# Optimization experiments

Measured on AMD Instinct MI355X. Metric: run time of the kernel, lower is better.

## Reference

```python
import jax, jax.numpy as jnp
import numpy as np

B, T, E = 4, 2048, 768
HN, HS = 12, 64          # head_num, head_size = E // HN
L = 6                    # n_layer
FF = 4 * E
O = 1                    # output_dim
EPS = 1e-5


def setup_inputs() -> dict:
    key = jax.random.key(0)
    ks = iter(jax.random.split(key, 40))
    r = lambda shape, s=0.02: jax.random.normal(next(ks), shape, jnp.float32) * s
    inp = {
        'idx': jax.random.normal(next(ks), (B, T, E), jnp.float32),
        'hidden': jnp.zeros((1, B, E), jnp.float32),
        # per-layer, per-head q/k/v linears
        'wq': r((L, HN, E, HS)), 'bq': jnp.zeros((L, HN, HS), jnp.float32),
        'wk': r((L, HN, E, HS)), 'bk': jnp.zeros((L, HN, HS), jnp.float32),
        'wv': r((L, HN, E, HS)), 'bv': jnp.zeros((L, HN, HS), jnp.float32),
        'wproj': r((L, E, E)), 'bproj': jnp.zeros((L, E), jnp.float32),
        'ln1_g': jnp.ones((L, E), jnp.float32), 'ln1_b': jnp.zeros((L, E), jnp.float32),
        'ln2_g': jnp.ones((L, E), jnp.float32), 'ln2_b': jnp.zeros((L, E), jnp.float32),
        'w1': r((L, E, FF)), 'b1': jnp.zeros((L, FF), jnp.float32),
        'w2': r((L, FF, E)), 'b2': jnp.zeros((L, E), jnp.float32),
        'lnf_g': jnp.ones((E,), jnp.float32), 'lnf_b': jnp.zeros((E,), jnp.float32),
        'fw1': r((E, FF)), 'fb1': jnp.zeros((FF,), jnp.float32),
        'fw2': r((FF, E)), 'fb2': jnp.zeros((E,), jnp.float32),
        'hw': r((E, O)), 'hb': jnp.zeros((O,), jnp.float32),
    }
    return inp


def _layernorm(x, g, b):
    m = jnp.mean(x, axis=-1, keepdims=True)
    v = jnp.var(x, axis=-1, keepdims=True)
    return (x - m) * jax.lax.rsqrt(v + EPS) * g + b


def _forward(idx, wq, bq, wk, bk, wv, bv, wproj, bproj,
             ln1_g, ln1_b, ln2_g, ln2_b, w1, b1, w2, b2,
             lnf_g, lnf_b, fw1, fb1, fw2, fb2, hw, hb):
    x = idx
    Bn, Tn, En = x.shape
    causal = jnp.tril(jnp.ones((Tn, Tn), bool))  # [T,T]
    scale = 1.0 / jnp.sqrt(jnp.asarray(En, x.dtype))  # NOTE: divides by sqrt(n_embed), as in source
    for l in range(wq.shape[0]):
        h = _layernorm(x, ln1_g[l], ln1_b[l])
        q = jnp.einsum('bte,hes->bhts', h, wq[l]) + bq[l][None, :, None, :]
        k = jnp.einsum('bte,hes->bhts', h, wk[l]) + bk[l][None, :, None, :]
        v = jnp.einsum('bte,hes->bhts', h, wv[l]) + bv[l][None, :, None, :]
        scores = jnp.einsum('bhts,bhus->bhtu', q, k) * scale
        scores = jnp.where(causal, scores, -jnp.inf)
        att = jax.nn.softmax(scores, axis=-1)
        o = jnp.einsum('bhtu,bhus->bhts', att, v)          # [B,HN,T,HS]
        o = o.transpose(0, 2, 1, 3).reshape(Bn, Tn, En)     # concat heads
        x = x + o @ wproj[l] + bproj[l]
        h = _layernorm(x, ln2_g[l], ln2_b[l])
        ff = jax.nn.gelu(h @ w1[l] + b1[l], approximate=False) @ w2[l] + b2[l]
        x = x + ff
    x = _layernorm(x, lnf_g, lnf_b)
    x = jax.nn.gelu(x @ fw1 + fb1, approximate=False) @ fw2 + fb2
    logits = x @ hw + hb            # [B,T,O]
    logits = logits[-1]             # [T,O]  (source: logits[-1,:,:])
    return jnp.squeeze(logits, axis=-1)  # [T]


def reference(idx, hidden, wq, bq, wk, bk, wv, bv, wproj, bproj,
              ln1_g, ln1_b, ln2_g, ln2_b, w1, b1, w2, b2,
              lnf_g, lnf_b, fw1, fb1, fw2, fb2, hw, hb):
    # hidden is accepted but unused by the original module.
    del hidden
    return _forward(idx, wq, bq, wk, bk, wv, bv, wproj, bproj,
                    ln1_g, ln1_b, ln2_g, ln2_b, w1, b1, w2, b2,
                    lnf_g, lnf_b, fw1, fb1, fw2, fb2, hw, hb)
```

## Files before the change

kernel.cpp:

```cpp
#include <hip/hip_runtime.h>
#include <math.h>

#define TT 2048
#define EE 768
#define HNN 12
#define HSS 64
#define NLAYER 6
#define FFD 3072
#define QKVN 2304

constexpr float LN_EPS = 1e-5f;
constexpr float ATT_SCALE = 0.03608439182435161f;

typedef __attribute__((ext_vector_type(8))) short bf16x8;
typedef __attribute__((ext_vector_type(4))) float f32x4;

__device__ __forceinline__ ushort f2bf(float f) {
    union { float f; uint u; } c; c.f = f;
    const uint u = c.u;
    return (ushort)((u + 0x7fffu + ((u >> 16) & 1u)) >> 16);
}

__device__ __forceinline__ void gload16(const void* g, void* l) {
    __builtin_amdgcn_global_load_lds((const __attribute__((address_space(1))) void*)g,
                                     (__attribute__((address_space(3))) void*)l, 16, 0, 0);
}

__global__ __launch_bounds__(256) void copy4_kernel(float4* __restrict__ dst,
                                                    const float4* __restrict__ src, int n4) {
    int i = blockIdx.x * 256 + threadIdx.x;
    if (i < n4) dst[i] = src[i];
}

__global__ __launch_bounds__(256) void ln_kernel(const float* __restrict__ in,
                                                 const float* __restrict__ g,
                                                 const float* __restrict__ b,
                                                 ushort* __restrict__ out) {
    __shared__ float red[8];
    const int t = blockIdx.x;
    const int tid = threadIdx.x;
    const float* row = in + (size_t)t * EE;
    float v0 = row[tid], v1 = row[tid + 256], v2 = row[tid + 512];
    float s = v0 + v1 + v2;
#pragma unroll
    for (int m = 1; m < 64; m <<= 1) s += __shfl_xor(s, m, 64);
    if ((tid & 63) == 0) red[tid >> 6] = s;
    __syncthreads();
    const float mean = (red[0] + red[1] + red[2] + red[3]) * (1.0f / EE);
    const float d0 = v0 - mean, d1 = v1 - mean, d2 = v2 - mean;
    float qq = d0 * d0 + d1 * d1 + d2 * d2;
#pragma unroll
    for (int m = 1; m < 64; m <<= 1) qq += __shfl_xor(qq, m, 64);
    __syncthreads();
    if ((tid & 63) == 0) red[tid >> 6] = qq;
    __syncthreads();
    const float var = (red[0] + red[1] + red[2] + red[3]) * (1.0f / EE);
    const float rstd = rsqrtf(var + LN_EPS);
    ushort* orow = out + (size_t)t * EE;
    orow[tid]       = f2bf(d0 * rstd * g[tid]       + b[tid]);
    orow[tid + 256] = f2bf(d1 * rstd * g[tid + 256] + b[tid + 256]);
    orow[tid + 512] = f2bf(d2 * rstd * g[tid + 512] + b[tid + 512]);
}

__device__ __forceinline__ void transpose64(const float* __restrict__ src, int sld,
                                            ushort* __restrict__ dst, int dld,
                                            int k0, int n0, int tid) {
    __shared__ float t[64][68];
#pragma unroll
    for (int p = 0; p < 4; p++) {
        const int kr = p * 16 + (tid >> 4);
        *(float4*)&t[kr][(tid & 15) * 4] =
            *(const float4*)&src[(size_t)(k0 + kr) * sld + n0 + (tid & 15) * 4];
    }
    __syncthreads();
#pragma unroll
    for (int q = 0; q < 2; q++) {
        const int nl = q * 32 + (tid >> 3);
        const int kc = (tid & 7) * 8;
        ushort v[8];
#pragma unroll
        for (int j = 0; j < 8; j++) v[j] = f2bf(t[kc + j][nl]);
        uint4 o;
        o.x = (uint)v[0] | ((uint)v[1] << 16);
        o.y = (uint)v[2] | ((uint)v[3] << 16);
        o.z = (uint)v[4] | ((uint)v[5] << 16);
        o.w = (uint)v[6] | ((uint)v[7] << 16);
        *(uint4*)&dst[(size_t)(n0 + nl) * dld + k0 + kc] = o;
    }
}

__global__ __launch_bounds__(256) void pack_t_kernel(const float* __restrict__ src, int sld,
                                                     ushort* __restrict__ dst, int dld) {
    transpose64(src, sld, dst, dld, blockIdx.x * 64, blockIdx.y * 64, threadIdx.x);
}

__global__ __launch_bounds__(256) void pack_qkv_kernel(const float* __restrict__ wq,
                                                       const float* __restrict__ wk,
                                                       const float* __restrict__ wv,
                                                       ushort* __restrict__ dst) {
    const int z = blockIdx.z;
    const int which = z / HNN, hd = z % HNN;
    const float* src = (which == 0 ? wq : which == 1 ? wk : wv) + (size_t)hd * EE * HSS;
    ushort* d = dst + (size_t)(which * EE + hd * HSS) * EE;
    transpose64(src, HSS, d, EE, blockIdx.x * 64, 0, threadIdx.x);
}

template <int EPI>
__global__ __launch_bounds__(256) void gemm_bf16(const ushort* __restrict__ A,
                                                 const ushort* __restrict__ Bt,
                                                 const float* __restrict__ b0,
                                                 const float* __restrict__ b1,
                                                 const float* __restrict__ b2,
                                                 float* __restrict__ outF,
                                                 ushort* __restrict__ outB,
                                                 int N, int K,
                                                 int nby, int KS, int Kslice) {
    __shared__ ushort Al[2][128 * 32];
    __shared__ ushort Bl[2][128 * 32];
    const int tid = threadIdx.x;
    const int wave = tid >> 6, lane = tid & 63;
    const int wm = wave >> 1, wn = wave & 1;
    const int l15 = lane & 15, q4 = lane >> 4;

    const int nwg = gridDim.x;
    const int wgid = ((int)blockIdx.x & 7) * (nwg >> 3) + ((int)blockIdx.x >> 3);
    const int mb = wgid % nby;
    const int t2 = wgid / nby;
    const int ks = t2 % KS;
    const int nb = t2 / KS;
    const int m0 = mb * 128, n0 = nb * 128;
    const int kbase = ks * Kslice;

    const int srow = lane >> 2;
    const int scb = (lane & 3) ^ ((lane >> 3) & 3);
    const ushort* Ag0 = A + (size_t)(m0 + wave * 16 + srow) * K + kbase + scb * 8;
    const ushort* Ag1 = Ag0 + (size_t)64 * K;
    const ushort* Bg0 = Bt + (size_t)(n0 + wave * 16 + srow) * K + kbase + scb * 8;
    const ushort* Bg1 = Bg0 + (size_t)64 * K;

    auto stage = [&](int buf, int kk) {
        const int off = kk * 32;
        gload16(Ag0 + off, &Al[buf][(wave * 16) * 32]);
        gload16(Ag1 + off, &Al[buf][(64 + wave * 16) * 32]);
        gload16(Bg0 + off, &Bl[buf][(wave * 16) * 32]);
        gload16(Bg1 + off, &Bl[buf][(64 + wave * 16) * 32]);
    };

    f32x4 acc[4][4];
#pragma unroll
    for (int i = 0; i < 4; i++)
#pragma unroll
        for (int j = 0; j < 4; j++) acc[i][j] = (f32x4){0.f, 0.f, 0.f, 0.f};

    stage(0, 0);
    __syncthreads();

    const int niter = Kslice >> 5;
    const int cq = (q4 ^ ((l15 >> 1) & 3)) * 8;

    for (int i = 0; i < niter; i++) {
        const int buf = i & 1;
        if (i + 1 < niter) stage(buf ^ 1, i + 1);
        bf16x8 af[4], bfr[4];
#pragma unroll
        for (int ii = 0; ii < 4; ii++)
            af[ii] = *(const bf16x8*)&Al[buf][(wm * 64 + ii * 16 + l15) * 32 + cq];
#pragma unroll
        for (int j = 0; j < 4; j++)
            bfr[j] = *(const bf16x8*)&Bl[buf][(wn * 64 + j * 16 + l15) * 32 + cq];
#pragma unroll
        for (int ii = 0; ii < 4; ii++)
#pragma unroll
            for (int j = 0; j < 4; j++)
                acc[ii][j] = __builtin_amdgcn_mfma_f32_16x16x32_bf16(af[ii], bfr[j], acc[ii][j], 0, 0, 0);
        __syncthreads();
    }

#pragma unroll
    for (int i = 0; i < 4; i++) {
        const int row = m0 + wm * 64 + i * 16 + q4 * 4;
#pragma unroll
        for (int j = 0; j < 4; j++) {
            const int col = n0 + wn * 64 + j * 16 + l15;
            float bias;
            if constexpr (EPI == 0)
                bias = (col < 768) ? b0[col] : (col < 1536 ? b1[col - 768] : b2[col - 1536]);
            else
                bias = (EPI == 1 && ks != 0) ? 0.f : b0[col];
#pragma unroll
            for (int r = 0; r < 4; r++) {
                const float v = acc[i][j][r] + bias;
                const size_t idx = (size_t)(row + r) * N + col;
                if constexpr (EPI == 0) {
                    outB[idx] = f2bf(v);
                } else if constexpr (EPI == 1) {
                    atomicAdd(&outF[idx], v);
                } else if constexpr (EPI == 2) {
                    outB[idx] = f2bf(0.5f * v * (1.0f + erff(v * 0.70710678118654752f)));
                } else {
                    outF[idx] = v;
                }
            }
        }
    }
}

__global__ __launch_bounds__(256) void attn_mfma(const ushort* __restrict__ qkv,
                                                 ushort* __restrict__ o_bf) {
    __shared__ __align__(16) ushort Ks[2][64 * 72];
    __shared__ __align__(16) ushort VT[2][64 * 72];
    __shared__ __align__(16) uint   Ps[4][16 * 36];

    const int bid = blockIdx.x;
    const int x = bid & 7, r = bid >> 3;
    int hd, qt;
    if (r < 32) { hd = x;            qt = 31 - r; }
    else        { hd = 8 + (x & 3);  qt = (r - 32) * 2 + (x >> 2); }

    const int tid = threadIdx.x;
    const int wave = tid >> 6, lane = tid & 63;
    const int l15 = lane & 15, q4 = lane >> 4;
    const int rw = tid >> 3;
    const int ch = tid & 7;

    bf16x8 qa0, qa1;
    {
        const ushort* qrow = qkv + (size_t)(qt * 64 + wave * 16 + l15) * QKVN + hd * 64;
        qa0 = *(const bf16x8*)&qrow[q4 * 8];
        qa1 = *(const bf16x8*)&qrow[32 + q4 * 8];
    }

    const ushort* kg = qkv + 768 + hd * 64 + ch * 8;
    const ushort* vg = qkv + 1536 + hd * 64 + ch * 8;

#pragma unroll
    for (int p = 0; p < 2; p++) {
        const int row = rw + p * 32;
        const uint4 kv = *(const uint4*)&kg[(size_t)row * QKVN];
        *(uint4*)&Ks[0][row * 72 + ch * 8] = kv;
        const uint4 w = *(const uint4*)&vg[(size_t)row * QKVN];
        const int swz = row ^ (ch << 3);
        ushort* vt = &VT[0][(ch * 8) * 72 + swz];
        vt[0 * 72] = (ushort)(w.x & 0xffff);
        vt[1 * 72] = (ushort)(w.x >> 16);
        vt[2 * 72] = (ushort)(w.y & 0xffff);
        vt[3 * 72] = (ushort)(w.y >> 16);
        vt[4 * 72] = (ushort)(w.z & 0xffff);
        vt[5 * 72] = (ushort)(w.z >> 16);
        vt[6 * 72] = (ushort)(w.w & 0xffff);
        vt[7 * 72] = (ushort)(w.w >> 16);
    }
    __syncthreads();

    float m_i = -1e30f;
    float l_i = 0.f;
    f32x4 oacc[4];
#pragma unroll
    for (int n = 0; n < 4; n++) oacc[n] = (f32x4){0.f, 0.f, 0.f, 0.f};

    for (int kt = 0; kt <= qt; kt++) {
        const int buf = kt & 1;
        const bool more = (kt < qt);
        uint4 knxt[2], vnxt[2];
        if (more) {
#pragma unroll
            for (int p = 0; p < 2; p++) {
                knxt[p] = *(const uint4*)&kg[(size_t)((kt + 1) * 64 + rw + p * 32) * QKVN];
                vnxt[p] = *(const uint4*)&vg[(size_t)((kt + 1) * 64 + rw + p * 32) * QKVN];
            }
        }

        const ushort* Kb = &Ks[buf][0];
        f32x4 s[4];
#pragma unroll
        for (int n = 0; n < 4; n++) {
            const bf16x8 kf0 = *(const bf16x8*)&Kb[(n * 16 + l15) * 72 + q4 * 8];
            const bf16x8 kf1 = *(const bf16x8*)&Kb[(n * 16 + l15) * 72 + 32 + q4 * 8];
            f32x4 a = (f32x4){0.f, 0.f, 0.f, 0.f};
            a = __builtin_amdgcn_mfma_f32_16x16x32_bf16(kf0, qa0, a, 0, 0, 0);
            a = __builtin_amdgcn_mfma_f32_16x16x32_bf16(kf1, qa1, a, 0, 0, 0);
            s[n] = a;
        }

        const bool diag = (kt == qt);
        const int qrl = wave * 16 + l15;
        float pe[16];
        float mx = -1e30f;
#pragma unroll
        for (int n = 0; n < 4; n++)
#pragma unroll
            for (int rr = 0; rr < 4; rr++) {
                float xv = s[n][rr] * ATT_SCALE;
                if (diag && (n * 16 + q4 * 4 + rr) > qrl) xv = -1e30f;
                pe[n * 4 + rr] = xv;
                mx = fmaxf(mx, xv);
            }
        mx = fmaxf(mx, __shfl_xor(mx, 16, 64));
        mx = fmaxf(mx, __shfl_xor(mx, 32, 64));
        const float nm = fmaxf(m_i, mx);
        const float al = __expf(m_i - nm);
        float rs = 0.f;
#pragma unroll
        for (int i = 0; i < 16; i++) {
            pe[i] = __expf(pe[i] - nm);
            rs += pe[i];
        }
        rs += __shfl_xor(rs, 16, 64);
        rs += __shfl_xor(rs, 32, 64);
        l_i = l_i * al + rs;
        m_i = nm;

        float alr[4];
#pragma unroll
        for (int rr = 0; rr < 4; rr++) alr[rr] = __shfl(al, q4 * 4 + rr, 64);
#pragma unroll
        for (int n = 0; n < 4; n++) {
            oacc[n][0] *= alr[0];
            oacc[n][1] *= alr[1];
            oacc[n][2] *= alr[2];
            oacc[n][3] *= alr[3];
        }

        uint* psrow = &Ps[wave][l15 * 36];
        const int psx = (l15 & 7) << 2;
#pragma unroll
        for (int n = 0; n < 4; n++) {
            uint2 d;
            d.x = (uint)f2bf(pe[n * 4 + 0]) | ((uint)f2bf(pe[n * 4 + 1]) << 16);
            d.y = (uint)f2bf(pe[n * 4 + 2]) | ((uint)f2bf(pe[n * 4 + 3]) << 16);
            *(uint2*)&psrow[(n * 8 + q4 * 2) ^ psx] = d;
        }
        const bf16x8 pa0 = *(const bf16x8*)&psrow[(q4 * 4) ^ psx];
        const bf16x8 pa1 = *(const bf16x8*)&psrow[(16 + q4 * 4) ^ psx];

        const ushort* Vb = &VT[buf][0];
#pragma unroll
        for (int n = 0; n < 4; n++) {
            const int drow = n * 16 + l15;
            const int vsw = ((drow >> 3) & 7) << 3;
            const bf16x8 vb0 = *(const bf16x8*)&Vb[drow * 72 + ((q4 * 8) ^ vsw)];
            const bf16x8 vb1 = *(const bf16x8*)&Vb[drow * 72 + ((32 + q4 * 8) ^ vsw)];
            oacc[n] = __builtin_amdgcn_mfma_f32_16x16x32_bf16(pa0, vb0, oacc[n], 0, 0, 0);
            oacc[n] = __builtin_amdgcn_mfma_f32_16x16x32_bf16(pa1, vb1, oacc[n], 0, 0, 0);
        }

        if (more) {
#pragma unroll
            for (int p = 0; p < 2; p++) {
                const int row = rw + p * 32;
                *(uint4*)&Ks[buf ^ 1][row * 72 + ch * 8] = knxt[p];
                const uint4 w = vnxt[p];
                const int swz = row ^ (ch << 3);
                ushort* vt = &VT[buf ^ 1][(ch * 8) * 72 + swz];
                vt[0 * 72] = (ushort)(w.x & 0xffff);
                vt[1 * 72] = (ushort)(w.x >> 16);
                vt[2 * 72] = (ushort)(w.y & 0xffff);
                vt[3 * 72] = (ushort)(w.y >> 16);
                vt[4 * 72] = (ushort)(w.z & 0xffff);
                vt[5 * 72] = (ushort)(w.z >> 16);
                vt[6 * 72] = (ushort)(w.w & 0xffff);
                vt[7 * 72] = (ushort)(w.w >> 16);
            }
        }
        __syncthreads();
    }

    float lrec[4];
#pragma unroll
    for (int rr = 0; rr < 4; rr++) lrec[rr] = 1.0f / __shfl(l_i, q4 * 4 + rr, 64);
#pragma unroll
    for (int n = 0; n < 4; n++)
#pragma unroll
        for (int rr = 0; rr < 4; rr++)
            o_bf[(size_t)(qt * 64 + wave * 16 + q4 * 4 + rr) * EE + hd * 64 + n * 16 + l15] =
                f2bf(oacc[n][rr] * lrec[rr]);
}

__global__ __launch_bounds__(256) void head_kernel(const float* __restrict__ x,
                                                   const float* __restrict__ hw,
                                                   const float* __restrict__ hb,
                                                   float* __restrict__ out) {
    __shared__ float red[8];
    const int t = blockIdx.x, tid = threadIdx.x;
    const float* row = x + (size_t)t * EE;
    float s = row[tid] * hw[tid] + row[tid + 256] * hw[tid + 256] + row[tid + 512] * hw[tid + 512];
#pragma unroll
    for (int m = 1; m < 64; m <<= 1) s += __shfl_xor(s, m, 64);
    if ((tid & 63) == 0) red[tid >> 6] = s;
    __syncthreads();
    if (tid == 0) out[t] = red[0] + red[1] + red[2] + red[3] + hb[0];
}

extern "C" void kernel_launch(void* const* d_in, const int* in_sizes, int n_in,
                              void* d_out, int out_size, void* d_ws, size_t ws_size,
                              hipStream_t stream) {
    const float* idx   = (const float*)d_in[0];
    const float* wq    = (const float*)d_in[2];
    const float* bq    = (const float*)d_in[3];
    const float* wk    = (const float*)d_in[4];
    const float* bk    = (const float*)d_in[5];
    const float* wv    = (const float*)d_in[6];
    const float* bv    = (const float*)d_in[7];
    const float* wproj = (const float*)d_in[8];
    const float* bproj = (const float*)d_in[9];
    const float* ln1g  = (const float*)d_in[10];
    const float* ln1b  = (const float*)d_in[11];
    const float* ln2g  = (const float*)d_in[12];
    const float* ln2b  = (const float*)d_in[13];
    const float* w1    = (const float*)d_in[14];
    const float* b1    = (const float*)d_in[15];
    const float* w2    = (const float*)d_in[16];
    const float* b2    = (const float*)d_in[17];
    const float* lnfg  = (const float*)d_in[18];
    const float* lnfb  = (const float*)d_in[19];
    const float* fw1   = (const float*)d_in[20];
    const float* fb1   = (const float*)d_in[21];
    const float* fw2   = (const float*)d_in[22];
    const float* fb2   = (const float*)d_in[23];
    const float* hw    = (const float*)d_in[24];
    const float* hb    = (const float*)d_in[25];
    float* out = (float*)d_out;

    char* p = (char*)d_ws;
    auto alloc = [&](size_t bytes) { void* r = (void*)p; p += (bytes + 255) & ~(size_t)255; return r; };
    float*  x     = (float*)alloc((size_t)TT * EE * 4);
    ushort* h_bf  = (ushort*)alloc((size_t)TT * EE * 2);
    ushort* qkvb  = (ushort*)alloc((size_t)TT * QKVN * 2);
    ushort* o_bf  = (ushort*)alloc((size_t)TT * EE * 2);
    ushort* ffb   = (ushort*)alloc((size_t)TT * FFD * 2);
    ushort* Wqkv  = (ushort*)alloc((size_t)QKVN * EE * 2);
    ushort* Wproj = (ushort*)alloc((size_t)EE * EE * 2);
    ushort* W1t   = (ushort*)alloc((size_t)FFD * EE * 2);
    ushort* W2t   = (ushort*)alloc((size_t)EE * FFD * 2);

    copy4_kernel<<<dim3((TT * EE / 4 + 255) / 256), dim3(256), 0, stream>>>(
        (float4*)x, (const float4*)(idx + (size_t)3 * TT * EE), TT * EE / 4);

    for (int l = 0; l < NLAYER; l++) {
        const size_t lw = (size_t)l;
        pack_qkv_kernel<<<dim3(12, 1, 36), dim3(256), 0, stream>>>(
            wq + lw * HNN * EE * HSS, wk + lw * HNN * EE * HSS, wv + lw * HNN * EE * HSS, Wqkv);
        pack_t_kernel<<<dim3(12, 12), dim3(256), 0, stream>>>(wproj + lw * EE * EE, EE, Wproj, EE);
        pack_t_kernel<<<dim3(12, 48), dim3(256), 0, stream>>>(w1 + lw * EE * FFD, FFD, W1t, EE);
        pack_t_kernel<<<dim3(48, 12), dim3(256), 0, stream>>>(w2 + lw * FFD * EE, EE, W2t, FFD);

        ln_kernel<<<dim3(TT), dim3(256), 0, stream>>>(x, ln1g + lw * EE, ln1b + lw * EE, h_bf);
        gemm_bf16<0><<<dim3(288), dim3(256), 0, stream>>>(
            h_bf, Wqkv, bq + lw * EE, bk + lw * EE, bv + lw * EE, nullptr, qkvb,
            QKVN, EE, 16, 1, EE);
        attn_mfma<<<dim3(384), dim3(256), 0, stream>>>(qkvb, o_bf);
        gemm_bf16<1><<<dim3(384), dim3(256), 0, stream>>>(
            o_bf, Wproj, bproj + lw * EE, nullptr, nullptr, x, nullptr,
            EE, EE, 16, 4, 192);
        ln_kernel<<<dim3(TT), dim3(256), 0, stream>>>(x, ln2g + lw * EE, ln2b + lw * EE, h_bf);
        gemm_bf16<2><<<dim3(384), dim3(256), 0, stream>>>(
            h_bf, W1t, b1 + lw * FFD, nullptr, nullptr, nullptr, ffb,
            FFD, EE, 16, 1, EE);
        gemm_bf16<1><<<dim3(384), dim3(256), 0, stream>>>(
            ffb, W2t, b2 + lw * EE, nullptr, nullptr, x, nullptr,
            EE, FFD, 16, 4, 768);
    }

    ln_kernel<<<dim3(TT), dim3(256), 0, stream>>>(x, lnfg, lnfb, h_bf);
    pack_t_kernel<<<dim3(12, 48), dim3(256), 0, stream>>>(fw1, FFD, W1t, EE);
    pack_t_kernel<<<dim3(48, 12), dim3(256), 0, stream>>>(fw2, EE, W2t, FFD);
    gemm_bf16<2><<<dim3(384), dim3(256), 0, stream>>>(
        h_bf, W1t, fb1, nullptr, nullptr, nullptr, ffb, FFD, EE, 16, 1, EE);
    gemm_bf16<3><<<dim3(96), dim3(256), 0, stream>>>(
        ffb, W2t, fb2, nullptr, nullptr, x, nullptr, EE, FFD, 16, 1, FFD);
    head_kernel<<<dim3(TT), dim3(256), 0, stream>>>(x, hw, hb, out);
}
```

Measured before the change: 1.548 ms.

## Pre-transpose V globally and make attention waves independent with register K/V streaming

Adds a separate kernel that writes V transposed per head into a global buffer. The attention kernel is restructured so each wave owns its own 16-row query tile and streams K and V^T fragments from global memory straight into registers, double-buffering K across iterations. This removes the shared-memory K/V staging and the block-wide barriers. It also switches softmax to exp2 with a prescaled log2e constant and uses tree reductions. The cost is one extra kernel launch per layer plus an extra pass over V. Global and L2 load traffic also rises, because each wave re-reads K/V on its own instead of sharing them within a block.

After: 1.620 ms. 4.7% more time.

```diff
diff --git a/kernel.cpp b/kernel.cpp
--- a/kernel.cpp
+++ b/kernel.cpp
@@ -11,6 +11,7 @@
 
 constexpr float LN_EPS = 1e-5f;
 constexpr float ATT_SCALE = 0.03608439182435161f;
+constexpr float ATT_SCALE_L2E = 0.03608439182435161f * 1.4426950408889634f;
 
 typedef __attribute__((ext_vector_type(8))) short bf16x8;
 typedef __attribute__((ext_vector_type(4))) float f32x4;
@@ -103,6 +104,25 @@
     const float* src = (which == 0 ? wq : which == 1 ? wk : wv) + (size_t)hd * EE * HSS;
     ushort* d = dst + (size_t)(which * EE + hd * HSS) * EE;
     transpose64(src, HSS, d, EE, blockIdx.x * 64, 0, threadIdx.x);
+}
+
+__global__ __launch_bounds__(256) void vtrans_kernel(const ushort* __restrict__ qkv,
+                                                     ushort* __restrict__ vT) {
+    const int t = blockIdx.x * 256 + threadIdx.x;
+    const int d = t & 63;
+    const int rest = t >> 6;
+    const int tb = rest & 255;
+    const int hd = rest >> 8;
+    const ushort* src = qkv + 1536 + hd * 64 + d;
+    ushort v[8];
+#pragma unroll
+    for (int j = 0; j < 8; j++) v[j] = src[(size_t)(tb * 8 + j) * QKVN];
+    uint4 o;
+    o.x = (uint)v[0] | ((uint)v[1] << 16);
+    o.y = (uint)v[2] | ((uint)v[3] << 16);
+    o.z = (uint)v[4] | ((uint)v[5] << 16);
+    o.w = (uint)v[6] | ((uint)v[7] << 16);
+    *(uint4*)&vT[((size_t)hd * 64 + d) * TT + tb * 8] = o;
 }
 
 template <int EPI>
@@ -205,111 +225,98 @@
     }
 }
 
-__global__ __launch_bounds__(256) void attn_mfma(const ushort* __restrict__ qkv,
-                                                 ushort* __restrict__ o_bf) {
-    __shared__ __align__(16) ushort Ks[2][64 * 72];
-    __shared__ __align__(16) ushort VT[2][64 * 72];
-    __shared__ __align__(16) uint   Ps[4][16 * 36];
-
-    const int bid = blockIdx.x;
-    const int x = bid & 7, r = bid >> 3;
-    int hd, qt;
-    if (r < 32) { hd = x;            qt = 31 - r; }
-    else        { hd = 8 + (x & 3);  qt = (r - 32) * 2 + (x >> 2); }
+__global__ __launch_bounds__(256, 2) void attn_mfma(const ushort* __restrict__ qkv,
+                                                    const ushort* __restrict__ vT,
+                                                    ushort* __restrict__ o_bf) {
+    __shared__ __align__(16) uint Ps[4][16 * 36];
 
     const int tid = threadIdx.x;
     const int wave = tid >> 6, lane = tid & 63;
     const int l15 = lane & 15, q4 = lane >> 4;
-    const int rw = tid >> 3;
-    const int ch = tid & 7;
-
-    bf16x8 qa0, qa1;
-    {
-        const ushort* qrow = qkv + (size_t)(qt * 64 + wave * 16 + l15) * QKVN + hd * 64;
-        qa0 = *(const bf16x8*)&qrow[q4 * 8];
-        qa1 = *(const bf16x8*)&qrow[32 + q4 * 8];
-    }
-
-    const ushort* kg = qkv + 768 + hd * 64 + ch * 8;
-    const ushort* vg = qkv + 1536 + hd * 64 + ch * 8;
-
-#pragma unroll
-    for (int p = 0; p < 2; p++) {
-        const int row = rw + p * 32;
-        const uint4 kv = *(const uint4*)&kg[(size_t)row * QKVN];
-        *(uint4*)&Ks[0][row * 72 + ch * 8] = kv;
-        const uint4 w = *(const uint4*)&vg[(size_t)row * QKVN];
-        const int swz = row ^ (ch << 3);
-        ushort* vt = &VT[0][(ch * 8) * 72 + swz];
-        vt[0 * 72] = (ushort)(w.x & 0xffff);
-        vt[1 * 72] = (ushort)(w.x >> 16);
-        vt[2 * 72] = (ushort)(w.y & 0xffff);
-        vt[3 * 72] = (ushort)(w.y >> 16);
-        vt[4 * 72] = (ushort)(w.z & 0xffff);
-        vt[5 * 72] = (ushort)(w.z >> 16);
-        vt[6 * 72] = (ushort)(w.w & 0xffff);
-        vt[7 * 72] = (ushort)(w.w >> 16);
-    }
-    __syncthreads();
-
-    float m_i = -1e30f;
-    float l_i = 0.f;
+
+    const int x = (int)blockIdx.x & 7, r = (int)blockIdx.x >> 3;
+    const int rho = wave * 48 + r;
+    int head, qi;
+    if (rho < 128) { head = x;           qi = 127 - rho; }
+    else           { head = 8 + (x >> 1); qi = 2 * (191 - rho) + (x & 1); }
+    const int nkt = (qi >> 2) + 1;
+    const int qrow_g = qi * 16 + l15;
+
+    const ushort* qp = qkv + (size_t)qrow_g * QKVN + head * 64;
+    const bf16x8 qa0 = *(const bf16x8*)&qp[q4 * 8];
+    const bf16x8 qa1 = *(const bf16x8*)&qp[32 + q4 * 8];
+
+    const ushort* kbase = qkv + 768 + head * 64 + (size_t)l15 * QKVN + q4 * 8;
+    const ushort* vbase = vT + ((size_t)head * 64 + l15) * TT + q4 * 8;
+
+    float m_i = -1e30f, l_i = 0.f;
     f32x4 oacc[4];
 #pragma unroll
     for (int n = 0; n < 4; n++) oacc[n] = (f32x4){0.f, 0.f, 0.f, 0.f};
 
-    for (int kt = 0; kt <= qt; kt++) {
-        const int buf = kt & 1;
-        const bool more = (kt < qt);
-        uint4 knxt[2], vnxt[2];
-        if (more) {
-#pragma unroll
-            for (int p = 0; p < 2; p++) {
-                knxt[p] = *(const uint4*)&kg[(size_t)((kt + 1) * 64 + rw + p * 32) * QKVN];
-                vnxt[p] = *(const uint4*)&vg[(size_t)((kt + 1) * 64 + rw + p * 32) * QKVN];
+    bf16x8 kA[8], kB[8], vC[8];
+#pragma unroll
+    for (int n = 0; n < 4; n++)
+#pragma unroll
+        for (int kb = 0; kb < 2; kb++)
+            kA[n * 2 + kb] = *(const bf16x8*)(kbase + (size_t)(n * 16) * QKVN + kb * 32);
+
+    uint* psrow = &Ps[wave][l15 * 36];
+
+    auto body = [&](bf16x8* kc, bf16x8* kn, int kt) {
+        const ushort* vp = vbase + kt * 64;
+#pragma unroll
+        for (int n = 0; n < 4; n++)
+#pragma unroll
+            for (int kb = 0; kb < 2; kb++)
+                vC[n * 2 + kb] = *(const bf16x8*)(vp + (size_t)(n * 16) * TT + kb * 32);
+        if (kt + 1 < nkt) {
+            const ushort* kp = kbase + (size_t)(kt + 1) * 64 * QKVN;
+#pragma unroll
+            for (int n = 0; n < 4; n++)
+#pragma unroll
+                for (int kb = 0; kb < 2; kb++)
+                    kn[n * 2 + kb] = *(const bf16x8*)(kp + (size_t)(n * 16) * QKVN + kb * 32);
+        }
+        f32x4 s[4];
+#pragma unroll
+        for (int n = 0; n < 4; n++) {
+            f32x4 a = (f32x4){0.f, 0.f, 0.f, 0.f};
+            a = __builtin_amdgcn_mfma_f32_16x16x32_bf16(kc[n * 2], qa0, a, 0, 0, 0);
+            a = __builtin_amdgcn_mfma_f32_16x16x32_bf16(kc[n * 2 + 1], qa1, a, 0, 0, 0);
+            s[n] = a;
+        }
+        float pe[16];
+        const bool diag = (kt == nkt - 1);
+#pragma unroll
+        for (int n = 0; n < 4; n++) {
+            const int k0 = kt * 64 + n * 16 + q4 * 4;
+#pragma unroll
+            for (int rr = 0; rr < 4; rr++) {
+                float xv = s[n][rr] * ATT_SCALE_L2E;
+                if (diag && (k0 + rr) > qrow_g) xv = -1e30f;
+                pe[n * 4 + rr] = xv;
             }
         }
-
-        const ushort* Kb = &Ks[buf][0];
-        f32x4 s[4];
-#pragma unroll
-        for (int n = 0; n < 4; n++) {
-            const bf16x8 kf0 = *(const bf16x8*)&Kb[(n * 16 + l15) * 72 + q4 * 8];
-            const bf16x8 kf1 = *(const bf16x8*)&Kb[(n * 16 + l15) * 72 + 32 + q4 * 8];
-            f32x4 a = (f32x4){0.f, 0.f, 0.f, 0.f};
-            a = __builtin_amdgcn_mfma_f32_16x16x32_bf16(kf0, qa0, a, 0, 0, 0);
-            a = __builtin_amdgcn_mfma_f32_16x16x32_bf16(kf1, qa1, a, 0, 0, 0);
-            s[n] = a;
-        }
-
-        const bool diag = (kt == qt);
-        const int qrl = wave * 16 + l15;
-        float pe[16];
-        float mx = -1e30f;
-#pragma unroll
-        for (int n = 0; n < 4; n++)
-#pragma unroll
-            for (int rr = 0; rr < 4; rr++) {
-                float xv = s[n][rr] * ATT_SCALE;
-                if (diag && (n * 16 + q4 * 4 + rr) > qrl) xv = -1e30f;
-                pe[n * 4 + rr] = xv;
-                mx = fmaxf(mx, xv);
-            }
+        float t8[8];
+#pragma unroll
+        for (int i = 0; i < 8; i++) t8[i] = fmaxf(pe[i], pe[i + 8]);
+        float mx = fmaxf(fmaxf(fmaxf(t8[0], t8[4]), fmaxf(t8[1], t8[5])),
+                         fmaxf(fmaxf(t8[2], t8[6]), fmaxf(t8[3], t8[7])));
         mx = fmaxf(mx, __shfl_xor(mx, 16, 64));
         mx = fmaxf(mx, __shfl_xor(mx, 32, 64));
         const float nm = fmaxf(m_i, mx);
-        const float al = __expf(m_i - nm);
-        float rs = 0.f;
-#pragma unroll
-        for (int i = 0; i < 16; i++) {
-            pe[i] = __expf(pe[i] - nm);
-            rs += pe[i];
-        }
+        const float al = exp2f(m_i - nm);
+#pragma unroll
+        for (int i = 0; i < 16; i++) pe[i] = exp2f(pe[i] - nm);
+        float s8[8];
+#pragma unroll
+        for (int i = 0; i < 8; i++) s8[i] = pe[i] + pe[i + 8];
+        float rs = ((s8[0] + s8[4]) + (s8[1] + s8[5])) + ((s8[2] + s8[6]) + (s8[3] + s8[7]));
         rs += __shfl_xor(rs, 16, 64);
         rs += __shfl_xor(rs, 32, 64);
         l_i = l_i * al + rs;
         m_i = nm;
-
         float alr[4];
 #pragma unroll
         for (int rr = 0; rr < 4; rr++) alr[rr] = __shfl(al, q4 * 4 + rr, 64);
@@ -320,49 +327,28 @@
             oacc[n][2] *= alr[2];
             oacc[n][3] *= alr[3];
         }
-
-        uint* psrow = &Ps[wave][l15 * 36];
-        const int psx = (l15 & 7) << 2;
 #pragma unroll
         for (int n = 0; n < 4; n++) {
-            uint2 d;
-            d.x = (uint)f2bf(pe[n * 4 + 0]) | ((uint)f2bf(pe[n * 4 + 1]) << 16);
-            d.y = (uint)f2bf(pe[n * 4 + 2]) | ((uint)f2bf(pe[n * 4 + 3]) << 16);
-            *(uint2*)&psrow[(n * 8 + q4 * 2) ^ psx] = d;
-        }
-        const bf16x8 pa0 = *(const bf16x8*)&psrow[(q4 * 4) ^ psx];
-        const bf16x8 pa1 = *(const bf16x8*)&psrow[(16 + q4 * 4) ^ psx];
-
-        const ushort* Vb = &VT[buf][0];
+            uint2 d2;
+            d2.x = (uint)f2bf(pe[n * 4 + 0]) | ((uint)f2bf(pe[n * 4 + 1]) << 16);
+            d2.y = (uint)f2bf(pe[n * 4 + 2]) | ((uint)f2bf(pe[n * 4 + 3]) << 16);
+            *(uint2*)&psrow[(8 * n + 2 * q4 + 4 * l15) & 31] = d2;
+        }
+        const bf16x8 pa0 = *(const bf16x8*)&psrow[(4 * q4 + 4 * l15) & 31];
+        const bf16x8 pa1 = *(const bf16x8*)&psrow[(16 + 4 * q4 + 4 * l15) & 31];
 #pragma unroll
         for (int n = 0; n < 4; n++) {
-            const int drow = n * 16 + l15;
-            const int vsw = ((drow >> 3) & 7) << 3;
-            const bf16x8 vb0 = *(const bf16x8*)&Vb[drow * 72 + ((q4 * 8) ^ vsw)];
-            const bf16x8 vb1 = *(const bf16x8*)&Vb[drow * 72 + ((32 + q4 * 8) ^ vsw)];
-            oacc[n] = __builtin_amdgcn_mfma_f32_16x16x32_bf16(pa0, vb0, oacc[n], 0, 0, 0);
-            oacc[n] = __builtin_amdgcn_mfma_f32_16x16x32_bf16(pa1, vb1, oacc[n], 0, 0, 0);
-        }
-
-        if (more) {
-#pragma unroll
-            for (int p = 0; p < 2; p++) {
-                const int row = rw + p * 32;
-                *(uint4*)&Ks[buf ^ 1][row * 72 + ch * 8] = knxt[p];
-                const uint4 w = vnxt[p];
-                const int swz = row ^ (ch << 3);
-                ushort* vt = &VT[buf ^ 1][(ch * 8) * 72 + swz];
-                vt[0 * 72] = (ushort)(w.x & 0xffff);
-                vt[1 * 72] = (ushort)(w.x >> 16);
-                vt[2 * 72] = (ushort)(w.y & 0xffff);
-                vt[3 * 72] = (ushort)(w.y >> 16);
-                vt[4 * 72] = (ushort)(w.z & 0xffff);
-                vt[5 * 72] = (ushort)(w.z >> 16);
-                vt[6 * 72] = (ushort)(w.w & 0xffff);
-                vt[7 * 72] = (ushort)(w.w >> 16);
-            }
-        }
-        __syncthreads();
+            oacc[n] = __builtin_amdgcn_mfma_f32_16x16x32_bf16(pa0, vC[n * 2], oacc[n], 0, 0, 0);
+            oacc[n] = __builtin_amdgcn_mfma_f32_16x16x32_bf16(pa1, vC[n * 2 + 1], oacc[n], 0, 0, 0);
+        }
+    };
+
+    int kt = 0;
+    for (;;) {
+        body(kA, kB, kt);
+        if (++kt >= nkt) break;
+        body(kB, kA, kt);
+        if (++kt >= nkt) break;
     }
 
     float lrec[4];
@@ -372,7 +358,7 @@
     for (int n = 0; n < 4; n++)
 #pragma unroll
         for (int rr = 0; rr < 4; rr++)
-            o_bf[(size_t)(qt * 64 + wave * 16 + q4 * 4 + rr) * EE + hd * 64 + n * 16 + l15] =
+            o_bf[(size_t)(qi * 16 + q4 * 4 + rr) * EE + head * 64 + n * 16 + l15] =
                 f2bf(oacc[n][rr] * lrec[rr]);
 }
 
@@ -432,6 +418,7 @@
     ushort* Wproj = (ushort*)alloc((size_t)EE * EE * 2);
     ushort* W1t   = (ushort*)alloc((size_t)FFD * EE * 2);
     ushort* W2t   = (ushort*)alloc((size_t)EE * FFD * 2);
+    ushort* vTb   = (ushort*)alloc((size_t)HNN * HSS * TT * 2);
 
     copy4_kernel<<<dim3((TT * EE / 4 + 255) / 256), dim3(256), 0, stream>>>(
         (float4*)x, (const float4*)(idx + (size_t)3 * TT * EE), TT * EE / 4);
@@ -448,7 +435,8 @@
         gemm_bf16<0><<<dim3(288), dim3(256), 0, stream>>>(
             h_bf, Wqkv, bq + lw * EE, bk + lw * EE, bv + lw * EE, nullptr, qkvb,
             QKVN, EE, 16, 1, EE);
-        attn_mfma<<<dim3(384), dim3(256), 0, stream>>>(qkvb, o_bf);
+        vtrans_kernel<<<dim3(768), dim3(256), 0, stream>>>(qkvb, vTb);
+        attn_mfma<<<dim3(384), dim3(256), 0, stream>>>(qkvb, vTb, o_bf);
         gemm_bf16<1><<<dim3(384), dim3(256), 0, stream>>>(
             o_bf, Wproj, bproj + lw * EE, nullptr, nullptr, x, nullptr,
             EE, EE, 16, 4, 192);
```
